# Kernel optimization log

Hardware: AMD Instinct MI355X
Metric: run time of the kernel (lower is better)

## Reference

```python
import jax, jax.numpy as jnp
import numpy as np
import math

B, NU, NA = 8, 256, 256
USER_DIM, ANT_DIM, EDGE_DIM = 128, 128, 64
HIDDEN, HEADS = 512, 8
HEAD_DIM = HIDDEN // HEADS  # 64
SLOPE = 0.2


def setup_inputs() -> dict:
    key = jax.random.key(0)
    ks = jax.random.split(key, 8)
    s = 0.05
    return {
        "user_feats": jax.random.normal(ks[0], (B, NU, USER_DIM), jnp.float32),
        "ant_feats": jax.random.normal(ks[1], (B, NA, ANT_DIM), jnp.float32),
        "edge_feats": jax.random.normal(ks[2], (B, NU, NA, EDGE_DIM), jnp.float32),
        # per-head projection weights, stored as [H, in_dim, head_dim] for x @ W
        "Wu": jax.random.normal(ks[3], (HEADS, USER_DIM, HEAD_DIM), jnp.float32) * s,
        "Wa": jax.random.normal(ks[4], (HEADS, ANT_DIM, HEAD_DIM), jnp.float32) * s,
        "We": jax.random.normal(ks[5], (HEADS, EDGE_DIM, HEAD_DIM), jnp.float32) * s,
        "av": jax.random.normal(ks[6], (HEADS, HEAD_DIM), jnp.float32) * s,
        "Wres": jax.random.normal(ks[7], (USER_DIM, HIDDEN), jnp.float32) * s,
    }


def reference(user_feats, ant_feats, edge_feats, Wu, Wa, We, av, Wres):
    scale = 1.0 / math.sqrt(HEAD_DIM)
    user_heads, ant_heads = [], []
    # loop over fixed small number of heads (mirrors module structure),
    # keeps the large [B,NU,NA,HEAD_DIM] intermediate to one head at a time
    for k in range(HEADS):
        U = user_feats @ Wu[k]          # [B,NU,hd]
        A = ant_feats @ Wa[k]           # [B,NA,hd]
        E = jnp.einsum('bune,ed->bund', edge_feats, We[k])  # [B,NU,NA,hd]
        S = U[:, :, None, :] + A[:, None, :, :] + E          # [B,NU,NA,hd]
        act = jnp.where(S >= 0, S, SLOPE * S)                # leaky relu 0.2
        score = jnp.einsum('bund,d->bun', act, av[k]) * scale
        alpha = jax.nn.softmax(score, axis=-1)               # over antennas
        # dropout p=0.3 is identity in eval mode
        aw = alpha[..., None]
        user_heads.append(((A[:, None, :, :] + E) * aw).sum(axis=2))  # [B,NU,hd]
        ant_heads.append(((U[:, :, None, :] + E) * aw).sum(axis=1))   # [B,NA,hd]
    user_out = jnp.concatenate(user_heads, axis=-1) + user_feats @ Wres
    ant_out = jnp.concatenate(ant_heads, axis=-1)
    return (user_out, ant_out)
```

## Files before the change

kernel.cpp:

```cpp
#include <hip/hip_runtime.h>
#include <math.h>

constexpr int B_  = 8;
constexpr int NU  = 256;
constexpr int NA  = 256;
constexpr int UD  = 128;
constexpr int ED  = 64;
constexpr int H   = 8;
constexpr int HD  = 64;
constexpr int HID = 512;
constexpr float SLOPE = 0.2f;
constexpr float SCALE = 0.125f;

constexpr size_t WS_UT    = 0;
constexpr size_t WS_AT    = 1048576;
constexpr size_t WS_UBASE = 2097152;
constexpr size_t WS_ALPHA = 3145728;
constexpr size_t WS_WET32 = 7340032;
constexpr size_t WS_WET16 = 7372800;

typedef __attribute__((ext_vector_type(8))) short short8v;
typedef __attribute__((ext_vector_type(4))) float f32x4;

static __device__ __forceinline__ unsigned short f2bf(float f) {
  unsigned int u = __float_as_uint(f);
  unsigned int r = (u + 0x7fffu + ((u >> 16) & 1u)) >> 16;
  return (unsigned short)r;
}

static __device__ __forceinline__ void block_sync_lds() {
  asm volatile("s_waitcnt lgkmcnt(0)" ::: "memory");
  __builtin_amdgcn_sched_barrier(0);
  __builtin_amdgcn_s_barrier();
  __builtin_amdgcn_sched_barrier(0);
}

template <int CTRL>
static __device__ __forceinline__ float dpp_add(float v) {
  return v + __int_as_float(__builtin_amdgcn_mov_dpp(
                 __float_as_int(v), CTRL, 0xF, 0xF, false));
}
static __device__ __forceinline__ float red16_dpp(float v) {
  v = dpp_add<0xB1>(v);
  v = dpp_add<0x4E>(v);
  v = dpp_add<0x141>(v);
  v = dpp_add<0x140>(v);
  return v;
}

__global__ __launch_bounds__(256) void prep_kernel(
    const float* __restrict__ user, const float* __restrict__ ant,
    const float* __restrict__ Wu, const float* __restrict__ Wa,
    const float* __restrict__ Wres, const float* __restrict__ We,
    float* __restrict__ ws)
{
  const int job = blockIdx.y;
  const int t   = threadIdx.x;
  __shared__ float xs[ED * HD];

  if (job == 3) {
    const int h = blockIdx.x;
    if (h >= H) return;
    const float4* src = (const float4*)(We + (size_t)h * ED * HD);
    #pragma unroll
    for (int i = 0; i < 4; ++i) ((float4*)xs)[i * 256 + t] = src[i * 256 + t];
    __syncthreads();
    const int d = t >> 2, q = t & 3;
    float* WeTf = ws + WS_WET32;
    unsigned short* WeT16 = (unsigned short*)(ws + WS_WET16);
    const size_t jrow = (size_t)(h * HD + d) * ED;
    #pragma unroll
    for (int k = 0; k < 16; ++k) {
      const int e = q * 16 + k;
      float v = xs[e * HD + d];
      WeTf[jrow + e]  = v;
      WeT16[jrow + e] = f2bf(v);
    }
    return;
  }

  const int r0  = blockIdx.x * 4;
  const int b   = r0 >> 8, lr = r0 & 255;

  const float* X = (job == 1) ? ant : user;
  const float* W = (job == 0) ? Wu : (job == 1) ? Wa : Wres;

  #pragma unroll
  for (int i = 0; i < 2; ++i) {
    int idx = i * 256 + t;
    xs[(idx >> 7) * UD + (idx & 127)] =
        X[(size_t)(r0 + (idx >> 7)) * UD + (idx & 127)];
  }
  __syncthreads();

  const int j0 = 2 * t;
  const float* wp;
  int wstride;
  if (job < 2) { wp = W + (size_t)(j0 >> 6) * (UD * HD) + (j0 & 63); wstride = HD; }
  else         { wp = W + j0;                                        wstride = HID; }

  float2 acc[4];
  #pragma unroll
  for (int r = 0; r < 4; ++r) acc[r] = make_float2(0.f, 0.f);

  for (int k = 0; k < UD; ++k) {
    float2 w = *(const float2*)(wp + (size_t)k * wstride);
    #pragma unroll
    for (int r = 0; r < 4; ++r) {
      float x = xs[r * UD + k];
      acc[r].x += x * w.x;
      acc[r].y += x * w.y;
    }
  }

  if (job < 2) {
    float* T = ws + (job == 0 ? WS_UT : WS_AT);
    float4 w0 = make_float4(acc[0].x, acc[1].x, acc[2].x, acc[3].x);
    float4 w1 = make_float4(acc[0].y, acc[1].y, acc[2].y, acc[3].y);
    *(float4*)(T + ((size_t)b * HID + j0)     * 256 + lr) = w0;
    *(float4*)(T + ((size_t)b * HID + j0 + 1) * 256 + lr) = w1;
  } else {
    float* outp = ws + WS_UBASE;
    #pragma unroll
    for (int r = 0; r < 4; ++r)
      *(float2*)(outp + (size_t)(r0 + r) * HID + j0) = acc[r];
  }
}

__global__ __launch_bounds__(512, 4) void score_user_kernel(
    const float* __restrict__ edge, const float* __restrict__ av,
    float* __restrict__ ws, float* __restrict__ out)
{
  const int bid = (blockIdx.x & 7) * 256 + (blockIdx.x >> 3);
  const int b = bid >> 8, u = bid & 255;
  const int t = threadIdx.x;

  __shared__ __align__(16) short ebuf[2][32 * ED];
  __shared__ float sc[NA * 9];
  __shared__ float gu[HID];
  __shared__ float sinv[H];

  const float* UT = ws + WS_UT;
  const float* AT = ws + WS_AT;

  const int w    = t >> 6;
  const int lane = t & 63;
  const int l16  = lane & 15;
  const int kgrp = lane >> 4;

  short8v wf[4][2];
  float   ucol[4];
  float   avv[4];
  const unsigned short* WeT16 = (const unsigned short*)(ws + WS_WET16);
  #pragma unroll
  for (int n = 0; n < 4; ++n) {
    const int j = 64 * w + 16 * n + l16;
    #pragma unroll
    for (int c = 0; c < 2; ++c)
      wf[n][c] = *(const short8v*)(WeT16 + (size_t)j * ED + c * 32 + kgrp * 8);
    ucol[n] = UT[((size_t)b * HID + j) * 256 + u];
    avv[n]  = av[j] * SCALE;
  }

  const float4* ep = (const float4*)(edge + (size_t)bid * NA * ED);
  const int srow = t >> 4, sc4 = t & 15;
  const int sbyte = (srow * 128 + sc4 * 8) ^ ((srow & 7) << 4);
  float4 v = ep[t];

  const float* ATbase = AT + (size_t)b * HID * 256 + kgrp * 4;

  float lsum = 0.f;
  float O[4] = {0.f, 0.f, 0.f, 0.f};

  for (int t8 = 0; t8 < 8; ++t8) {
    const int cur = t8 & 1;
    {
      unsigned int lo, hi;
      asm("v_cvt_pk_bf16_f32 %0, %1, %2" : "=v"(lo) : "v"(v.x), "v"(v.y));
      asm("v_cvt_pk_bf16_f32 %0, %1, %2" : "=v"(hi) : "v"(v.z), "v"(v.w));
      *(uint2*)((char*)ebuf[cur] + sbyte) = make_uint2(lo, hi);
    }

    const int a0 = t8 * 32;
    f32x4 acc[2][4];
    #pragma unroll
    for (int m = 0; m < 2; ++m)
      #pragma unroll
      for (int n = 0; n < 4; ++n) {
        const int j = 64 * w + 16 * n + l16;
        float4 a4 = *(const float4*)(ATbase + (size_t)j * 256 + a0 + m * 16);
        f32x4 vv; vv[0] = a4.x; vv[1] = a4.y; vv[2] = a4.z; vv[3] = a4.w;
        acc[m][n] = vv;
      }

    __builtin_amdgcn_sched_barrier(0);

    if (t8 < 7) v = ep[(t8 + 1) * 512 + t];

    block_sync_lds();

    short8v af[2][2];
    #pragma unroll
    for (int m = 0; m < 2; ++m) {
      #pragma unroll
      for (int c = 0; c < 2; ++c) {
        int row = m * 16 + l16;
        int byte = (row * 128 + (c * 32 + kgrp * 8) * 2) ^ ((row & 7) << 4);
        af[m][c] = *(const short8v*)((const char*)ebuf[cur] + byte);
      }
    }

    #pragma unroll
    for (int c = 0; c < 2; ++c)
      #pragma unroll
      for (int m = 0; m < 2; ++m)
        #pragma unroll
        for (int n = 0; n < 4; ++n)
          acc[m][n] = __builtin_amdgcn_mfma_f32_16x16x32_bf16(
              af[m][c], wf[n][c], acc[m][n], 0, 0, 0);

    #pragma unroll
    for (int m = 0; m < 2; ++m) {
      #pragma unroll
      for (int q = 0; q < 4; ++q) {
        float h0 = 0.f;
        #pragma unroll
        for (int n = 0; n < 4; ++n) {
          float s = acc[m][n][q] + ucol[n];
          float sl = fmaxf(s, SLOPE * s);
          h0 = fmaf(sl, avv[n], h0);
        }
        h0 = red16_dpp(h0);
        float e = __expf(h0);
        lsum += e;
        if (l16 == 0) sc[(a0 + m * 16 + kgrp * 4 + q) * 9 + w] = e;
        #pragma unroll
        for (int n = 0; n < 4; ++n) O[n] += e * acc[m][n][q];
      }
    }
  }

  lsum += __shfl_xor(lsum, 16);
  lsum += __shfl_xor(lsum, 32);
  #pragma unroll
  for (int n = 0; n < 4; ++n) {
    O[n] += __shfl_xor(O[n], 16);
    O[n] += __shfl_xor(O[n], 32);
  }
  const float inv = 1.0f / lsum;

  if (lane == 0) sinv[w] = inv;
  if (kgrp == 0) {
    #pragma unroll
    for (int n = 0; n < 4; ++n) gu[w * 64 + n * 16 + l16] = O[n] * inv;
  }
  __syncthreads();

  {
    float* ag = ws + WS_ALPHA + (size_t)bid * (NA * H);
    #pragma unroll
    for (int i = 0; i < 4; ++i) {
      int idx = i * 512 + t;
      int a = idx >> 3, hh = idx & 7;
      ag[idx] = sc[a * 9 + hh] * sinv[hh];
    }
  }
  out[(size_t)bid * HID + t] = gu[t] + ws[WS_UBASE + (size_t)bid * HID + t];
}

__global__ __launch_bounds__(512, 4) void ant_kernel(
    const float* __restrict__ edge, float* __restrict__ ws,
    float* __restrict__ out)
{
  const int bid = (blockIdx.x & 7) * 64 + (blockIdx.x >> 3);
  const int b = bid >> 6, a0 = (bid & 63) * 4;
  const int t = threadIdx.x;
  const int w = t >> 6;
  const int lane = t & 63;

  __shared__ float plds[NU * 36];
  __shared__ float galds[4 * H * ED];

  {
    const float4* ag4 = (const float4*)(ws + WS_ALPHA) +
                        ((size_t)b * NU * NA * H) / 4 + a0 * 2;
    #pragma unroll
    for (int r = 0; r < 4; ++r) {
      int idx4 = r * 512 + t;
      int uu = idx4 >> 3, f = idx4 & 7;
      float4 vv = ag4[(size_t)uu * (NA * H / 4) + f];
      float* dst = plds + uu * 36 + (f & 1) * 16 + (f >> 1);
      dst[0]  = vv.x;
      dst[4]  = vv.y;
      dst[8]  = vv.z;
      dst[12] = vv.w;
    }
  }
  __syncthreads();

  const int u_loc = lane >> 4, e4 = lane & 15;
  float4 g[4] = {{0,0,0,0},{0,0,0,0},{0,0,0,0},{0,0,0,0}};

  {
    const float* ebase0 = edge + (((size_t)b * NU) * NA + a0) * ED + e4 * 4;

    float4 ce0, ce1, ce2, ce3, cp;
    {
      const float* eb = ebase0 + (size_t)u_loc * (NA * ED);
      ce0 = *(const float4*)(eb);
      ce1 = *(const float4*)(eb + ED);
      ce2 = *(const float4*)(eb + 2 * ED);
      ce3 = *(const float4*)(eb + 3 * ED);
      cp  = *(const float4*)(plds + u_loc * 36 + w * 4);
    }

    for (int u0 = 0; u0 < NU; u0 += 4) {
      const int un = (u0 + 4 < NU ? u0 + 4 : u0) + u_loc;
      const float* eb = ebase0 + (size_t)un * (NA * ED);
      float4 ne0 = *(const float4*)(eb);
      float4 ne1 = *(const float4*)(eb + ED);
      float4 ne2 = *(const float4*)(eb + 2 * ED);
      float4 ne3 = *(const float4*)(eb + 3 * ED);
      float4 np  = *(const float4*)(plds + un * 36 + w * 4);

      g[0].x += cp.x * ce0.x; g[0].y += cp.x * ce0.y; g[0].z += cp.x * ce0.z; g[0].w += cp.x * ce0.w;
      g[1].x += cp.y * ce1.x; g[1].y += cp.y * ce1.y; g[1].z += cp.y * ce1.z; g[1].w += cp.y * ce1.w;
      g[2].x += cp.z * ce2.x; g[2].y += cp.z * ce2.y; g[2].z += cp.z * ce2.z; g[2].w += cp.z * ce2.w;
      g[3].x += cp.w * ce3.x; g[3].y += cp.w * ce3.y; g[3].z += cp.w * ce3.z; g[3].w += cp.w * ce3.w;

      ce0 = ne0; ce1 = ne1; ce2 = ne2; ce3 = ne3; cp = np;
    }
  }
  #pragma unroll
  for (int al = 0; al < 4; ++al) {
    g[al].x += __shfl_xor(g[al].x, 16); g[al].x += __shfl_xor(g[al].x, 32);
    g[al].y += __shfl_xor(g[al].y, 16); g[al].y += __shfl_xor(g[al].y, 32);
    g[al].z += __shfl_xor(g[al].z, 16); g[al].z += __shfl_xor(g[al].z, 32);
    g[al].w += __shfl_xor(g[al].w, 16); g[al].w += __shfl_xor(g[al].w, 32);
  }
  if (u_loc == 0) {
    #pragma unroll
    for (int al = 0; al < 4; ++al)
      *(float4*)(galds + (al * H + w) * ED + e4 * 4) = g[al];
  }

  float pu[4] = {0.f, 0.f, 0.f, 0.f};
  {
    const float* UTj = ws + WS_UT + ((size_t)b * HID + t) * 256;
    for (int u0 = 0; u0 < NU; u0 += 4) {
      float4 U4 = *(const float4*)(UTj + u0);
      float4 p0 = *(const float4*)(plds + (u0 + 0) * 36 + w * 4);
      float4 p1 = *(const float4*)(plds + (u0 + 1) * 36 + w * 4);
      float4 p2 = *(const float4*)(plds + (u0 + 2) * 36 + w * 4);
      float4 p3 = *(const float4*)(plds + (u0 + 3) * 36 + w * 4);
      pu[0] += p0.x*U4.x + p1.x*U4.y + p2.x*U4.z + p3.x*U4.w;
      pu[1] += p0.y*U4.x + p1.y*U4.y + p2.y*U4.z + p3.y*U4.w;
      pu[2] += p0.z*U4.x + p1.z*U4.y + p2.z*U4.z + p3.z*U4.w;
      pu[3] += p0.w*U4.x + p1.w*U4.y + p2.w*U4.z + p3.w*U4.w;
    }
  }
  __syncthreads();

  {
    const float* wrow = ws + WS_WET32 + (size_t)t * ED;
    float o[4] = {pu[0], pu[1], pu[2], pu[3]};
    for (int e0 = 0; e0 < ED; e0 += 4) {
      float4 wv = *(const float4*)(wrow + e0);
      #pragma unroll
      for (int al = 0; al < 4; ++al) {
        float4 ga4 = *(const float4*)(galds + (al * H + w) * ED + e0);
        o[al] += ga4.x*wv.x + ga4.y*wv.y + ga4.z*wv.z + ga4.w*wv.w;
      }
    }
    float* outa = out + (size_t)(B_ * NU) * HID;
    #pragma unroll
    for (int al = 0; al < 4; ++al)
      outa[(size_t)((b * NA) + a0 + al) * HID + t] = o[al];
  }
}

extern "C" void kernel_launch(void* const* d_in, const int* in_sizes, int n_in,
                              void* d_out, int out_size, void* d_ws, size_t ws_size,
                              hipStream_t stream) {
  const float* user = (const float*)d_in[0];
  const float* ant  = (const float*)d_in[1];
  const float* edge = (const float*)d_in[2];
  const float* Wu   = (const float*)d_in[3];
  const float* Wa   = (const float*)d_in[4];
  const float* We   = (const float*)d_in[5];
  const float* av   = (const float*)d_in[6];
  const float* Wres = (const float*)d_in[7];
  float* out = (float*)d_out;
  float* ws  = (float*)d_ws;

  prep_kernel<<<dim3(512, 4), 256, 0, stream>>>(user, ant, Wu, Wa, Wres, We, ws);
  score_user_kernel<<<dim3(B_ * NU), 512, 0, stream>>>(edge, av, ws, out);
  ant_kernel<<<dim3(B_ * 64), 512, 0, stream>>>(edge, ws, out);
}
```

Baseline: 249.4 us.

## Split score_user kernel across two blocks per user, four heads each

The score/user kernel now launches two blocks per (batch, user) row, each covering four heads. Each head is split across two waves of 32 output columns, and their partial scores are summed through LDS before the exponent and the weighted sum. The per-wave MFMA tile and register footprint shrink, the occupancy hint in launch bounds is removed, and the edge tile drops to a single LDS buffer. In exchange, every edge row is loaded and converted to bf16 twice, and an extra block-wide barrier runs in each tile iteration.

```diff
diff --git a/kernel.cpp b/kernel.cpp
--- a/kernel.cpp
+++ b/kernel.cpp
@@ -127,34 +127,42 @@
   }
 }
 
-__global__ __launch_bounds__(512, 4) void score_user_kernel(
+__global__ __launch_bounds__(512) void score_user_kernel(
     const float* __restrict__ edge, const float* __restrict__ av,
     float* __restrict__ ws, float* __restrict__ out)
 {
-  const int bid = (blockIdx.x & 7) * 256 + (blockIdx.x >> 3);
-  const int b = bid >> 8, u = bid & 255;
-  const int t = threadIdx.x;
-
-  __shared__ __align__(16) short ebuf[2][32 * ED];
-  __shared__ float sc[NA * 9];
-  __shared__ float gu[HID];
-  __shared__ float sinv[H];
-
-  const float* UT = ws + WS_UT;
-  const float* AT = ws + WS_AT;
+  const int raw  = blockIdx.x;
+  const int b    = raw & 7;
+  const int rest = raw >> 3;
+  const int u    = rest >> 1;
+  const int p    = rest & 1;
+  const int bid  = b * NU + u;
+  const int t    = threadIdx.x;
+
+  __shared__ __align__(16) short ebuf[32 * ED];
+  __shared__ float sc[NA * 5];
+  __shared__ float part[4][2][32];
+  __shared__ float gu[256];
+  __shared__ float sinv[4];
 
   const int w    = t >> 6;
   const int lane = t & 63;
   const int l16  = lane & 15;
   const int kgrp = lane >> 4;
-
-  short8v wf[4][2];
-  float   ucol[4];
-  float   avv[4];
+  const int hl   = w >> 1;
+  const int half = w & 1;
+  const int jbase = 256 * p + 64 * hl + 32 * half;
+
+  const float* UT = ws + WS_UT;
+  const float* AT = ws + WS_AT;
+
+  short8v wf[2][2];
+  float   ucol[2];
+  float   avv[2];
   const unsigned short* WeT16 = (const unsigned short*)(ws + WS_WET16);
   #pragma unroll
-  for (int n = 0; n < 4; ++n) {
-    const int j = 64 * w + 16 * n + l16;
+  for (int n = 0; n < 2; ++n) {
+    const int j = jbase + 16 * n + l16;
     #pragma unroll
     for (int c = 0; c < 2; ++c)
       wf[n][c] = *(const short8v*)(WeT16 + (size_t)j * ED + c * 32 + kgrp * 8);
@@ -170,54 +178,46 @@
   const float* ATbase = AT + (size_t)b * HID * 256 + kgrp * 4;
 
   float lsum = 0.f;
-  float O[4] = {0.f, 0.f, 0.f, 0.f};
+  float O[2] = {0.f, 0.f};
 
   for (int t8 = 0; t8 < 8; ++t8) {
-    const int cur = t8 & 1;
     {
       unsigned int lo, hi;
       asm("v_cvt_pk_bf16_f32 %0, %1, %2" : "=v"(lo) : "v"(v.x), "v"(v.y));
       asm("v_cvt_pk_bf16_f32 %0, %1, %2" : "=v"(hi) : "v"(v.z), "v"(v.w));
-      *(uint2*)((char*)ebuf[cur] + sbyte) = make_uint2(lo, hi);
+      *(uint2*)((char*)ebuf + sbyte) = make_uint2(lo, hi);
     }
 
     const int a0 = t8 * 32;
-    f32x4 acc[2][4];
+    f32x4 acc[2][2];
     #pragma unroll
     for (int m = 0; m < 2; ++m)
       #pragma unroll
-      for (int n = 0; n < 4; ++n) {
-        const int j = 64 * w + 16 * n + l16;
+      for (int n = 0; n < 2; ++n) {
+        const int j = jbase + 16 * n + l16;
         float4 a4 = *(const float4*)(ATbase + (size_t)j * 256 + a0 + m * 16);
         f32x4 vv; vv[0] = a4.x; vv[1] = a4.y; vv[2] = a4.z; vv[3] = a4.w;
         acc[m][n] = vv;
       }
 
     __builtin_amdgcn_sched_barrier(0);
-
     if (t8 < 7) v = ep[(t8 + 1) * 512 + t];
 
     block_sync_lds();
 
-    short8v af[2][2];
     #pragma unroll
     for (int m = 0; m < 2; ++m) {
-      #pragma unroll
-      for (int c = 0; c < 2; ++c) {
-        int row = m * 16 + l16;
-        int byte = (row * 128 + (c * 32 + kgrp * 8) * 2) ^ ((row & 7) << 4);
-        af[m][c] = *(const short8v*)((const char*)ebuf[cur] + byte);
-      }
-    }
-
-    #pragma unroll
-    for (int c = 0; c < 2; ++c)
-      #pragma unroll
-      for (int m = 0; m < 2; ++m)
-        #pragma unroll
-        for (int n = 0; n < 4; ++n)
-          acc[m][n] = __builtin_amdgcn_mfma_f32_16x16x32_bf16(
-              af[m][c], wf[n][c], acc[m][n], 0, 0, 0);
+      const int row = m * 16 + l16;
+      const int bx = (row & 7) << 4;
+      short8v af0 = *(const short8v*)((const char*)ebuf +
+                     ((row * 128 + kgrp * 16) ^ bx));
+      short8v af1 = *(const short8v*)((const char*)ebuf +
+                     ((row * 128 + 64 + kgrp * 16) ^ bx));
+      acc[m][0] = __builtin_amdgcn_mfma_f32_16x16x32_bf16(af0, wf[0][0], acc[m][0], 0, 0, 0);
+      acc[m][1] = __builtin_amdgcn_mfma_f32_16x16x32_bf16(af0, wf[1][0], acc[m][1], 0, 0, 0);
+      acc[m][0] = __builtin_amdgcn_mfma_f32_16x16x32_bf16(af1, wf[0][1], acc[m][0], 0, 0, 0);
+      acc[m][1] = __builtin_amdgcn_mfma_f32_16x16x32_bf16(af1, wf[1][1], acc[m][1], 0, 0, 0);
+    }
 
     #pragma unroll
     for (int m = 0; m < 2; ++m) {
@@ -225,47 +225,60 @@
       for (int q = 0; q < 4; ++q) {
         float h0 = 0.f;
         #pragma unroll
-        for (int n = 0; n < 4; ++n) {
+        for (int n = 0; n < 2; ++n) {
           float s = acc[m][n][q] + ucol[n];
           float sl = fmaxf(s, SLOPE * s);
           h0 = fmaf(sl, avv[n], h0);
         }
         h0 = red16_dpp(h0);
-        float e = __expf(h0);
+        if (l16 == 0) part[hl][half][m * 16 + kgrp * 4 + q] = h0;
+      }
+    }
+
+    block_sync_lds();
+
+    #pragma unroll
+    for (int m = 0; m < 2; ++m) {
+      #pragma unroll
+      for (int q = 0; q < 4; ++q) {
+        const int al = m * 16 + kgrp * 4 + q;
+        float hs = part[hl][0][al] + part[hl][1][al];
+        float e = __expf(hs);
         lsum += e;
-        if (l16 == 0) sc[(a0 + m * 16 + kgrp * 4 + q) * 9 + w] = e;
-        #pragma unroll
-        for (int n = 0; n < 4; ++n) O[n] += e * acc[m][n][q];
+        if (half == 0 && l16 == 0) sc[(a0 + al) * 5 + hl] = e;
+        O[0] += e * acc[m][0][q];
+        O[1] += e * acc[m][1][q];
       }
     }
   }
 
   lsum += __shfl_xor(lsum, 16);
   lsum += __shfl_xor(lsum, 32);
-  #pragma unroll
-  for (int n = 0; n < 4; ++n) {
-    O[n] += __shfl_xor(O[n], 16);
-    O[n] += __shfl_xor(O[n], 32);
-  }
+  O[0] += __shfl_xor(O[0], 16);  O[0] += __shfl_xor(O[0], 32);
+  O[1] += __shfl_xor(O[1], 16);  O[1] += __shfl_xor(O[1], 32);
   const float inv = 1.0f / lsum;
 
-  if (lane == 0) sinv[w] = inv;
+  if (half == 0 && lane == 0) sinv[hl] = inv;
   if (kgrp == 0) {
     #pragma unroll
-    for (int n = 0; n < 4; ++n) gu[w * 64 + n * 16 + l16] = O[n] * inv;
+    for (int n = 0; n < 2; ++n)
+      gu[64 * hl + 32 * half + 16 * n + l16] = O[n] * inv;
   }
   __syncthreads();
 
   {
-    float* ag = ws + WS_ALPHA + (size_t)bid * (NA * H);
-    #pragma unroll
-    for (int i = 0; i < 4; ++i) {
+    float* ag = ws + WS_ALPHA + (size_t)bid * (NA * H) + p * 4;
+    #pragma unroll
+    for (int i = 0; i < 2; ++i) {
       int idx = i * 512 + t;
-      int a = idx >> 3, hh = idx & 7;
-      ag[idx] = sc[a * 9 + hh] * sinv[hh];
-    }
-  }
-  out[(size_t)bid * HID + t] = gu[t] + ws[WS_UBASE + (size_t)bid * HID + t];
+      int a = idx >> 2, hh = idx & 3;
+      ag[(size_t)a * H + hh] = sc[a * 5 + hh] * sinv[hh];
+    }
+  }
+  if (t < 256) {
+    const size_t o = (size_t)bid * HID + 256 * p + t;
+    out[o] = gu[t] + ws[WS_UBASE + o];
+  }
 }
 
 __global__ __launch_bounds__(512, 4) void ant_kernel(
@@ -394,6 +407,6 @@
   float* ws  = (float*)d_ws;
 
   prep_kernel<<<dim3(512, 4), 256, 0, stream>>>(user, ant, Wu, Wa, Wres, We, ws);
-  score_user_kernel<<<dim3(B_ * NU), 512, 0, stream>>>(edge, av, ws, out);
+  score_user_kernel<<<dim3(2 * B_ * NU), 512, 0, stream>>>(edge, av, ws, out);
   ant_kernel<<<dim3(B_ * 64), 512, 0, stream>>>(edge, ws, out);
 }
```

After: 272.8 us. 9.4% more time.
